# Kernel optimization log

Hardware: AMD Instinct MI355X
Metric: run time of the kernel (lower is better)

Reference implementation:

```python
import jax, jax.numpy as jnp
import numpy as np

HIDDEN_DIM = 2048
NUM_HEADS = 16
HEAD_DIM = HIDDEN_DIM // NUM_HEADS


def setup_inputs() -> dict:
    key = jax.random.key(0)
    ks = jax.random.split(key, 5)
    B, S, D = 1, 2048, HIDDEN_DIM
    scale = 1.0 / np.sqrt(D)
    return {
        "x": jax.random.normal(ks[0], (B, S, D), dtype=jnp.float32),
        "w_q": jax.random.normal(ks[1], (D, D), dtype=jnp.float32) * scale,
        "w_k": jax.random.normal(ks[2], (D, D), dtype=jnp.float32) * scale,
        "w_v": jax.random.normal(ks[3], (D, D), dtype=jnp.float32) * scale,
        "w_o": jax.random.normal(ks[4], (D, D), dtype=jnp.float32) * scale,
    }


def reference(x, w_q, w_k, w_v, w_o):
    # x: (B, S, D). Projections use x @ W.T as in the torch module.
    B, S, D = x.shape
    H, Hd = NUM_HEADS, HEAD_DIM
    q = (x @ w_q.T).reshape(B, S, H, Hd)
    k = (x @ w_k.T).reshape(B, S, H, Hd)
    v = (x @ w_v.T).reshape(B, S, H, Hd)
    scale = 1.0 / np.sqrt(Hd).astype(np.float32)
    # The tiled online-softmax loop computes exact softmax attention.
    scores = jnp.einsum("bqhd,bkhd->bhqk", q, k) * scale  # (B,H,S,S)
    p = jax.nn.softmax(scores, axis=-1)
    o = jnp.einsum("bhqk,bkhd->bqhd", p, v).reshape(B, S, D)
    return o @ w_o.T
```

## Files before the change

### kernel.cpp

```cpp
#include <hip/hip_runtime.h>
#include <hip/hip_bf16.h>
#include <cstdint>
#include <cstddef>

typedef __bf16 bf16x8 __attribute__((ext_vector_type(8)));
typedef float f32x4 __attribute__((ext_vector_type(4)));
typedef float f32x16 __attribute__((ext_vector_type(16)));
typedef unsigned short u16x8 __attribute__((ext_vector_type(8)));
typedef unsigned short u16x4 __attribute__((ext_vector_type(4)));

#define S_LEN 2048
#define DMODEL 2048
#define NHEADS 16
#define HD 128

__device__ inline unsigned short f2bf(float f) {
  union { float f; unsigned int u; } v; v.f = f;
  unsigned int r = (v.u + 0x7fffu + ((v.u >> 16) & 1u)) >> 16;
  return (unsigned short)r;
}

__device__ __forceinline__ void gload16(const unsigned short* g,
                                        unsigned short* lds) {
  __builtin_amdgcn_global_load_lds(
      (const __attribute__((address_space(1))) void*)g,
      (__attribute__((address_space(3))) void*)lds, 16, 0, 0);
}

__global__ void cast_all(const float* __restrict__ x, const float* __restrict__ wq,
                         const float* __restrict__ wk, const float* __restrict__ wv,
                         const float* __restrict__ wo,
                         unsigned short* __restrict__ out, float qscale) {
  const int b = blockIdx.x;
  const int seg = b >> 12;
  const int i = ((b & 4095) * 256 + threadIdx.x) * 4;
  const float* src = seg == 0 ? x : seg == 1 ? wq : seg == 2 ? wk
                   : seg == 3 ? wv : wo;
  const float scale = (seg == 1) ? qscale : 1.0f;
  unsigned short* dst = out + (size_t)seg * ((size_t)S_LEN * DMODEL);
  float4 v = *(const float4*)(src + i);
  u16x4 o;
  o.x = f2bf(v.x * scale); o.y = f2bf(v.y * scale);
  o.z = f2bf(v.z * scale); o.w = f2bf(v.w * scale);
  *(u16x4*)(dst + i) = o;
}

template <int MODE>
__device__ __forceinline__ void gemm_core64(
    const unsigned short* __restrict__ A, const unsigned short* __restrict__ B,
    unsigned short* __restrict__ Cb,
    int M, int N, int K, int m0, int n0,
    unsigned short* As, unsigned short* Bs) {
  constexpr int BK = 64;
  const int tid = threadIdx.x;
  const int wave = tid >> 6, lane = tid & 63;
  const int lg = lane >> 4, lr = lane & 15;
  const int rw = (wave >> 1) * 64;
  const int cw = (wave & 1) * 64;
  const int swz = lr & 7;

  const unsigned short* Ap[4];
  const unsigned short* Bp[4];
  unsigned short *as[4], *bs[4];
#pragma unroll
  for (int j = 0; j < 4; j++) {
    const int cc = j * 256 + tid;
    const int row = cc >> 3;
    const int col8 = (cc & 7) ^ (row & 7);
    Ap[j] = A + (size_t)(m0 + row) * K + col8 * 8;
    Bp[j] = B + (size_t)(n0 + row) * K + col8 * 8;
    as[j] = As + j * 2048 + wave * 512;
    bs[j] = Bs + j * 2048 + wave * 512;
  }

  f32x4 acc[4][4];
#pragma unroll
  for (int i = 0; i < 4; i++)
#pragma unroll
    for (int j = 0; j < 4; j++) acc[i][j] = (f32x4){0.f, 0.f, 0.f, 0.f};

  const int nk = K / BK;
  for (int kt = 0; kt < nk; ++kt) {
    const int ko = kt * BK;
    __syncthreads();
#pragma unroll
    for (int j = 0; j < 4; j++) {
      gload16(Ap[j] + ko, as[j]);
      gload16(Bp[j] + ko, bs[j]);
    }
    __syncthreads();

#pragma unroll
    for (int kk = 0; kk < 2; kk++) {
      bf16x8 af[4], bfr[4];
#pragma unroll
      for (int mt = 0; mt < 4; mt++)
        af[mt] = *(const bf16x8*)(As + (rw + mt * 16 + lr) * 64 +
                                  (((kk * 4 + lg) ^ swz) * 8));
#pragma unroll
      for (int nt = 0; nt < 4; nt++)
        bfr[nt] = *(const bf16x8*)(Bs + (cw + nt * 16 + lr) * 64 +
                                   (((kk * 4 + lg) ^ swz) * 8));
#pragma unroll
      for (int mt = 0; mt < 4; mt++)
#pragma unroll
        for (int nt = 0; nt < 4; nt++)
          acc[mt][nt] = __builtin_amdgcn_mfma_f32_16x16x32_bf16(
              af[mt], bfr[nt], acc[mt][nt], 0, 0, 0);
    }
  }

#pragma unroll
  for (int mt = 0; mt < 4; mt++)
#pragma unroll
    for (int nt = 0; nt < 4; nt++) {
      const int col = n0 + cw + nt * 16 + lr;
#pragma unroll
      for (int r = 0; r < 4; r++) {
        const int row = m0 + rw + mt * 16 + lg * 4 + r;
        const float v = acc[mt][nt][r];
        if (MODE == 1) Cb[(size_t)row * N + col] = f2bf(v);
        else Cb[(size_t)col * M + row] = f2bf(v);
      }
    }
}

__global__ __launch_bounds__(256, 2) void gemm_qkv(
    const unsigned short* __restrict__ xb, const unsigned short* __restrict__ wqb,
    const unsigned short* __restrict__ wkb, const unsigned short* __restrict__ wvb,
    unsigned short* __restrict__ qb, unsigned short* __restrict__ kb,
    unsigned short* __restrict__ vTb) {
  __shared__ unsigned short As[128 * 64];
  __shared__ unsigned short Bs[128 * 64];
  const int which = blockIdx.x >> 4;
  const int n0 = (blockIdx.x & 15) * 128;
  const int m0 = blockIdx.y * 128;
  if (which == 0)
    gemm_core64<1>(xb, wqb, qb, S_LEN, DMODEL, DMODEL, m0, n0, As, Bs);
  else if (which == 1)
    gemm_core64<1>(xb, wkb, kb, S_LEN, DMODEL, DMODEL, m0, n0, As, Bs);
  else
    gemm_core64<2>(xb, wvb, vTb, S_LEN, DMODEL, DMODEL, m0, n0, As, Bs);
}

__global__ __launch_bounds__(256, 2) void gemm_bt64(
    const unsigned short* __restrict__ A, const unsigned short* __restrict__ B,
    float* __restrict__ Cf, int M, int N, int K) {
  constexpr int BK = 128;
  __shared__ unsigned short As[64 * 128];
  __shared__ unsigned short Bs[128 * 128];
  const int tid = threadIdx.x;
  const int wave = tid >> 6, lane = tid & 63;
  const int lg = lane >> 4, lr = lane & 15;
  const int rw = (wave >> 1) * 32;
  const int cw = (wave & 1) * 64;
  const int m0 = blockIdx.y * 64, n0 = blockIdx.x * 128;
  const int swz = lr & 7;

  const unsigned short* Ap[4];
  const unsigned short* Bp[8];
  unsigned short *as[4], *bs[8];
#pragma unroll
  for (int j = 0; j < 4; j++) {
    const int cc = j * 256 + tid;
    const int row = cc >> 4;
    const int col16 = (cc & 15) ^ (row & 7);
    Ap[j] = A + (size_t)(m0 + row) * K + col16 * 8;
    as[j] = As + j * 2048 + wave * 512;
  }
#pragma unroll
  for (int j = 0; j < 8; j++) {
    const int cc = j * 256 + tid;
    const int row = cc >> 4;
    const int col16 = (cc & 15) ^ (row & 7);
    Bp[j] = B + (size_t)(n0 + row) * K + col16 * 8;
    bs[j] = Bs + j * 2048 + wave * 512;
  }

  f32x4 acc[2][4];
#pragma unroll
  for (int i = 0; i < 2; i++)
#pragma unroll
    for (int j = 0; j < 4; j++) acc[i][j] = (f32x4){0.f, 0.f, 0.f, 0.f};

  const int nk = K / BK;
  for (int kt = 0; kt < nk; ++kt) {
    const int ko = kt * BK;
    __syncthreads();
#pragma unroll
    for (int j = 0; j < 4; j++) gload16(Ap[j] + ko, as[j]);
#pragma unroll
    for (int j = 0; j < 8; j++) gload16(Bp[j] + ko, bs[j]);
    __syncthreads();

#pragma unroll
    for (int kk = 0; kk < 4; kk++) {
      bf16x8 af[2], bfr[4];
#pragma unroll
      for (int mt = 0; mt < 2; mt++)
        af[mt] = *(const bf16x8*)(As + (rw + mt * 16 + lr) * 128 +
                                  (((kk * 4 + lg) ^ swz) * 8));
#pragma unroll
      for (int nt = 0; nt < 4; nt++)
        bfr[nt] = *(const bf16x8*)(Bs + (cw + nt * 16 + lr) * 128 +
                                   (((kk * 4 + lg) ^ swz) * 8));
#pragma unroll
      for (int mt = 0; mt < 2; mt++)
#pragma unroll
        for (int nt = 0; nt < 4; nt++)
          acc[mt][nt] = __builtin_amdgcn_mfma_f32_16x16x32_bf16(
              af[mt], bfr[nt], acc[mt][nt], 0, 0, 0);
    }
  }

#pragma unroll
  for (int mt = 0; mt < 2; mt++)
#pragma unroll
    for (int nt = 0; nt < 4; nt++) {
      const int col = n0 + cw + nt * 16 + lr;
#pragma unroll
      for (int r = 0; r < 4; r++) {
        const int row = m0 + rw + mt * 16 + lg * 4 + r;
        Cf[(size_t)row * N + col] = acc[mt][nt][r];
      }
    }
}

__global__ __launch_bounds__(256, 2) void attn_kernel(
    const unsigned short* __restrict__ q, const unsigned short* __restrict__ k,
    const unsigned short* __restrict__ vT, unsigned short* __restrict__ o) {
  constexpr int KT = 64;
  __shared__ unsigned short Ks[2][64 * 136];
  __shared__ unsigned short Vt[128 * 72];
  __shared__ unsigned short Ps[64 * 72];
  __shared__ float Lred[4][32];

  const int tid = threadIdx.x;
  const int w = tid >> 6, lane = tid & 63;
  const int l32 = lane & 31, lh = lane >> 5;
  const int qh = w >> 1;
  const int kh = w & 1;
  const int h = blockIdx.y;
  const int q0 = blockIdx.x * 64;

  bf16x8 qf[8];
#pragma unroll
  for (int ks = 0; ks < 8; ks++)
    qf[ks] = *(const bf16x8*)(q + (size_t)(q0 + qh * 32 + l32) * DMODEL +
                              h * HD + ks * 16 + lh * 8);

  f32x16 Oacc[2];
#pragma unroll
  for (int mt = 0; mt < 2; mt++)
#pragma unroll
    for (int j = 0; j < 16; j++) Oacc[mt][j] = 0.f;
  f32x4 lsumv = (f32x4){0.f, 0.f, 0.f, 0.f};

  int krow[4], kcg[4], vrow[4], vcg[4];
#pragma unroll
  for (int i = 0; i < 4; i++) {
    const int c = i * 256 + tid;
    krow[i] = c >> 4; kcg[i] = c & 15;
    vrow[i] = c >> 3; vcg[i] = c & 7;
  }

  u16x8 kreg[4], vreg[4];
#pragma unroll
  for (int i = 0; i < 4; i++) {
    kreg[i] = *(const u16x8*)(k + (size_t)(krow[i]) * DMODEL + h * HD + kcg[i] * 8);
    vreg[i] = *(const u16x8*)(vT + (size_t)(h * HD + vrow[i]) * S_LEN + vcg[i] * 8);
  }
#pragma unroll
  for (int i = 0; i < 4; i++)
    *(u16x8*)(Ks[0] + krow[i] * 136 + kcg[i] * 8) = kreg[i];
  __syncthreads();

  constexpr int NT = S_LEN / KT;
  for (int kt = 0; kt < NT; ++kt) {
#pragma unroll
    for (int i = 0; i < 4; i++)
      *(u16x8*)(Vt + vrow[i] * 72 + vcg[i] * 8) = vreg[i];

    if (kt + 1 < NT) {
      const int kbase = (kt + 1) * KT;
#pragma unroll
      for (int i = 0; i < 4; i++) {
        kreg[i] = *(const u16x8*)(k + (size_t)(kbase + krow[i]) * DMODEL +
                                  h * HD + kcg[i] * 8);
        vreg[i] = *(const u16x8*)(vT + (size_t)(h * HD + vrow[i]) * S_LEN +
                                  kbase + vcg[i] * 8);
      }
    }

    const unsigned short* Kcur = Ks[kt & 1];
    bf16x8 kf[8];
#pragma unroll
    for (int ks = 0; ks < 8; ks++)
      kf[ks] = *(const bf16x8*)(Kcur + (kh * 32 + l32) * 136 + ks * 16 + lh * 8);

    f32x16 sacc0, sacc1;
#pragma unroll
    for (int j = 0; j < 16; j++) { sacc0[j] = 0.f; sacc1[j] = 0.f; }
    __builtin_amdgcn_s_setprio(1);
#pragma unroll
    for (int ks = 0; ks < 4; ks++) {
      sacc0 = __builtin_amdgcn_mfma_f32_32x32x16_bf16(kf[ks], qf[ks], sacc0,
                                                      0, 0, 0);
      sacc1 = __builtin_amdgcn_mfma_f32_32x32x16_bf16(kf[ks + 4], qf[ks + 4],
                                                      sacc1, 0, 0, 0);
    }
    __builtin_amdgcn_s_setprio(0);
    const f32x16 sacc = sacc0 + sacc1;

#pragma unroll
    for (int rq = 0; rq < 4; rq++) {
      u16x4 pk;
#pragma unroll
      for (int ri = 0; ri < 4; ri++) {
        const float p = __builtin_amdgcn_exp2f(sacc[rq * 4 + ri]);
        lsumv[ri] += p;
        union { float f; unsigned int u; } cv; cv.f = p;
        pk[ri] = (unsigned short)(cv.u >> 16);
      }
      *(u16x4*)(Ps + (qh * 32 + l32) * 72 + kh * 32 + rq * 8 + lh * 4) = pk;
    }

    if (kt + 1 < NT) {
#pragma unroll
      for (int i = 0; i < 4; i++)
        *(u16x8*)(Ks[(kt + 1) & 1] + krow[i] * 136 + kcg[i] * 8) = kreg[i];
    }
    __syncthreads();

    bf16x8 pfr[4], vf[2][4];
#pragma unroll
    for (int ks2 = 0; ks2 < 4; ks2++)
      pfr[ks2] =
          *(const bf16x8*)(Ps + (qh * 32 + l32) * 72 + ks2 * 16 + lh * 8);
#pragma unroll
    for (int ks2 = 0; ks2 < 4; ks2++)
#pragma unroll
      for (int mt = 0; mt < 2; mt++)
        vf[mt][ks2] = *(const bf16x8*)(
            Vt + (kh * 64 + mt * 32 + l32) * 72 + ks2 * 16 + lh * 8);

    __builtin_amdgcn_s_setprio(1);
#pragma unroll
    for (int ks2 = 0; ks2 < 4; ks2++)
#pragma unroll
      for (int mt = 0; mt < 2; mt++)
        Oacc[mt] = __builtin_amdgcn_mfma_f32_32x32x16_bf16(
            vf[mt][ks2], pfr[ks2], Oacc[mt], 0, 0, 0);
    __builtin_amdgcn_s_setprio(0);
    __syncthreads();
  }

  float lsum = (lsumv[0] + lsumv[1]) + (lsumv[2] + lsumv[3]);
  lsum += __shfl_xor(lsum, 32);
  if (lh == 0) Lred[w][l32] = lsum;
  __syncthreads();
  const float ltot = Lred[qh * 2][l32] + Lred[qh * 2 + 1][l32];
  const float inv = 1.0f / ltot;

#pragma unroll
  for (int mt = 0; mt < 2; mt++)
#pragma unroll
    for (int rq = 0; rq < 4; rq++) {
      u16x4 pk;
#pragma unroll
      for (int ri = 0; ri < 4; ri++)
        pk[ri] = f2bf(Oacc[mt][rq * 4 + ri] * inv);
      *(u16x4*)(Ks[0] + (qh * 32 + l32) * 136 + kh * 64 + mt * 32 + rq * 8 +
                lh * 4) = pk;
    }
  __syncthreads();
#pragma unroll
  for (int i = 0; i < 4; i++) {
    const int c = i * 256 + tid;
    const int row = c >> 4, ch = c & 15;
    const u16x8 vv = *(const u16x8*)(Ks[0] + row * 136 + ch * 8);
    *(u16x8*)(o + (size_t)(q0 + row) * DMODEL + h * HD + ch * 8) = vv;
  }
}

extern "C" void kernel_launch(void* const* d_in, const int* in_sizes, int n_in,
                              void* d_out, int out_size, void* d_ws, size_t ws_size,
                              hipStream_t stream) {
  (void)in_sizes; (void)n_in; (void)out_size; (void)ws_size;
  const float* x  = (const float*)d_in[0];
  const float* wq = (const float*)d_in[1];
  const float* wk = (const float*)d_in[2];
  const float* wv = (const float*)d_in[3];
  const float* wo = (const float*)d_in[4];
  float* out = (float*)d_out;

  const size_t NE = (size_t)S_LEN * DMODEL;
  unsigned short* ws = (unsigned short*)d_ws;
  unsigned short* xb  = ws + 0 * NE;
  unsigned short* wqb = ws + 1 * NE;
  unsigned short* wkb = ws + 2 * NE;
  unsigned short* wvb = ws + 3 * NE;
  unsigned short* wob = ws + 4 * NE;
  unsigned short* qb  = ws + 5 * NE;
  unsigned short* kb  = ws + 6 * NE;
  unsigned short* vTb = ws + 7 * NE;
  unsigned short* ob  = ws + 8 * NE;

  const float qscale = 0.08838834764831845f * 1.4426950408889634f;

  cast_all<<<dim3(5 * 4096), dim3(256), 0, stream>>>(x, wq, wk, wv, wo, ws,
                                                     qscale);

  gemm_qkv<<<dim3(48, 16), dim3(256), 0, stream>>>(xb, wqb, wkb, wvb, qb, kb,
                                                   vTb);

  attn_kernel<<<dim3(S_LEN / 64, NHEADS), dim3(256), 0, stream>>>(qb, kb, vTb,
                                                                  ob);

  gemm_bt64<<<dim3(16, 32), dim3(256), 0, stream>>>(ob, wob, out, S_LEN,
                                                    DMODEL, DMODEL);
}
```

Before: 251.3 us.

## Keep P in registers via permlane swap, split keys across waves, swizzle LDS

```diff
diff --git a/kernel.cpp b/kernel.cpp
--- a/kernel.cpp
+++ b/kernel.cpp
@@ -231,13 +231,13 @@
     const unsigned short* __restrict__ vT, unsigned short* __restrict__ o) {
   constexpr int KT = 64;
   __shared__ unsigned short Ks[2][64 * 136];
-  __shared__ unsigned short Vt[128 * 72];
-  __shared__ unsigned short Ps[64 * 72];
+  __shared__ unsigned short Vt[2][128 * 72];
   __shared__ float Lred[4][32];
 
   const int tid = threadIdx.x;
   const int w = tid >> 6, lane = tid & 63;
   const int l32 = lane & 31, lh = lane >> 5;
+  const int l7 = l32 & 7;
   const int qh = w >> 1;
   const int kh = w & 1;
   const int h = blockIdx.y;
@@ -249,20 +249,33 @@
     qf[ks] = *(const bf16x8*)(q + (size_t)(q0 + qh * 32 + l32) * DMODEL +
                               h * HD + ks * 16 + lh * 8);
 
-  f32x16 Oacc[2];
-#pragma unroll
-  for (int mt = 0; mt < 2; mt++)
+  f32x16 Oacc[4];
+#pragma unroll
+  for (int mt = 0; mt < 4; mt++)
 #pragma unroll
     for (int j = 0; j < 16; j++) Oacc[mt][j] = 0.f;
   f32x4 lsumv = (f32x4){0.f, 0.f, 0.f, 0.f};
 
-  int krow[4], kcg[4], vrow[4], vcg[4];
+  int krow[4], kcg[4], vrow[4], vcg[4], kso[4], vso[4];
 #pragma unroll
   for (int i = 0; i < 4; i++) {
     const int c = i * 256 + tid;
     krow[i] = c >> 4; kcg[i] = c & 15;
     vrow[i] = c >> 3; vcg[i] = c & 7;
-  }
+    kso[i] = krow[i] * 136 + (kcg[i] ^ (krow[i] & 7)) * 8;
+    vso[i] = vrow[i] * 72 + (vcg[i] ^ (vrow[i] & 7)) * 8;
+  }
+
+  int kfo[8];
+#pragma unroll
+  for (int ks = 0; ks < 8; ks++)
+    kfo[ks] = (kh * 32 + l32) * 136 + (((ks * 2 + lh) ^ l7) * 8);
+  int vfo[4][2];
+#pragma unroll
+  for (int mt = 0; mt < 4; mt++)
+#pragma unroll
+    for (int s = 0; s < 2; s++)
+      vfo[mt][s] = (mt * 32 + l32) * 72 + (((kh * 4 + s * 2 + lh) ^ l7) * 8);
 
   u16x8 kreg[4], vreg[4];
 #pragma unroll
@@ -271,16 +284,14 @@
     vreg[i] = *(const u16x8*)(vT + (size_t)(h * HD + vrow[i]) * S_LEN + vcg[i] * 8);
   }
 #pragma unroll
-  for (int i = 0; i < 4; i++)
-    *(u16x8*)(Ks[0] + krow[i] * 136 + kcg[i] * 8) = kreg[i];
+  for (int i = 0; i < 4; i++) {
+    *(u16x8*)(Ks[0] + kso[i]) = kreg[i];
+    *(u16x8*)(Vt[0] + vso[i]) = vreg[i];
+  }
   __syncthreads();
 
   constexpr int NT = S_LEN / KT;
   for (int kt = 0; kt < NT; ++kt) {
-#pragma unroll
-    for (int i = 0; i < 4; i++)
-      *(u16x8*)(Vt + vrow[i] * 72 + vcg[i] * 8) = vreg[i];
-
     if (kt + 1 < NT) {
       const int kbase = (kt + 1) * KT;
 #pragma unroll
@@ -292,93 +303,105 @@
       }
     }
 
-    const unsigned short* Kcur = Ks[kt & 1];
-    bf16x8 kf[8];
-#pragma unroll
-    for (int ks = 0; ks < 8; ks++)
-      kf[ks] = *(const bf16x8*)(Kcur + (kh * 32 + l32) * 136 + ks * 16 + lh * 8);
-
+    const unsigned short* Kb = Ks[kt & 1];
     f32x16 sacc0, sacc1;
 #pragma unroll
     for (int j = 0; j < 16; j++) { sacc0[j] = 0.f; sacc1[j] = 0.f; }
     __builtin_amdgcn_s_setprio(1);
 #pragma unroll
     for (int ks = 0; ks < 4; ks++) {
-      sacc0 = __builtin_amdgcn_mfma_f32_32x32x16_bf16(kf[ks], qf[ks], sacc0,
-                                                      0, 0, 0);
-      sacc1 = __builtin_amdgcn_mfma_f32_32x32x16_bf16(kf[ks + 4], qf[ks + 4],
-                                                      sacc1, 0, 0, 0);
+      const bf16x8 kf0 = *(const bf16x8*)(Kb + kfo[ks]);
+      const bf16x8 kf1 = *(const bf16x8*)(Kb + kfo[ks + 4]);
+      sacc0 = __builtin_amdgcn_mfma_f32_32x32x16_bf16(kf0, qf[ks], sacc0, 0, 0, 0);
+      sacc1 = __builtin_amdgcn_mfma_f32_32x32x16_bf16(kf1, qf[ks + 4], sacc1, 0, 0, 0);
     }
     __builtin_amdgcn_s_setprio(0);
     const f32x16 sacc = sacc0 + sacc1;
 
-#pragma unroll
-    for (int rq = 0; rq < 4; rq++) {
-      u16x4 pk;
-#pragma unroll
-      for (int ri = 0; ri < 4; ri++) {
-        const float p = __builtin_amdgcn_exp2f(sacc[rq * 4 + ri]);
-        lsumv[ri] += p;
-        union { float f; unsigned int u; } cv; cv.f = p;
-        pk[ri] = (unsigned short)(cv.u >> 16);
+    float p[16];
+#pragma unroll
+    for (int r = 0; r < 16; r++) p[r] = __builtin_amdgcn_exp2f(sacc[r]);
+#pragma unroll
+    for (int r = 0; r < 4; r++)
+      lsumv[r] += (p[4 * r] + p[4 * r + 1]) + (p[4 * r + 2] + p[4 * r + 3]);
+
+    unsigned int Aw[8];
+#pragma unroll
+    for (int i = 0; i < 8; i++)
+      asm("v_cvt_pk_bf16_f32 %0, %1, %2"
+          : "=v"(Aw[i]) : "v"(p[2 * i]), "v"(p[2 * i + 1]));
+    asm volatile("v_permlane32_swap_b32 %0, %1" : "+v"(Aw[0]), "+v"(Aw[2]));
+    asm volatile("v_permlane32_swap_b32 %0, %1" : "+v"(Aw[1]), "+v"(Aw[3]));
+    asm volatile("v_permlane32_swap_b32 %0, %1" : "+v"(Aw[4]), "+v"(Aw[6]));
+    asm volatile("v_permlane32_swap_b32 %0, %1" : "+v"(Aw[5]), "+v"(Aw[7]));
+    union { unsigned int wd[4]; bf16x8 v; } u0, u1;
+    u0.wd[0] = Aw[0]; u0.wd[1] = Aw[1]; u0.wd[2] = Aw[2]; u0.wd[3] = Aw[3];
+    u1.wd[0] = Aw[4]; u1.wd[1] = Aw[5]; u1.wd[2] = Aw[6]; u1.wd[3] = Aw[7];
+    const bf16x8 pfr0 = u0.v, pfr1 = u1.v;
+
+    const unsigned short* Vb = Vt[kt & 1];
+    __builtin_amdgcn_s_setprio(1);
+#pragma unroll
+    for (int mt = 0; mt < 4; mt++) {
+      const bf16x8 v0 = *(const bf16x8*)(Vb + vfo[mt][0]);
+      const bf16x8 v1 = *(const bf16x8*)(Vb + vfo[mt][1]);
+      Oacc[mt] = __builtin_amdgcn_mfma_f32_32x32x16_bf16(v0, pfr0, Oacc[mt], 0, 0, 0);
+      Oacc[mt] = __builtin_amdgcn_mfma_f32_32x32x16_bf16(v1, pfr1, Oacc[mt], 0, 0, 0);
+    }
+    __builtin_amdgcn_s_setprio(0);
+
+    if (kt + 1 < NT) {
+      unsigned short* Kn = Ks[(kt + 1) & 1];
+      unsigned short* Vn = Vt[(kt + 1) & 1];
+#pragma unroll
+      for (int i = 0; i < 4; i++) {
+        *(u16x8*)(Kn + kso[i]) = kreg[i];
+        *(u16x8*)(Vn + vso[i]) = vreg[i];
       }
-      *(u16x4*)(Ps + (qh * 32 + l32) * 72 + kh * 32 + rq * 8 + lh * 4) = pk;
-    }
-
-    if (kt + 1 < NT) {
-#pragma unroll
-      for (int i = 0; i < 4; i++)
-        *(u16x8*)(Ks[(kt + 1) & 1] + krow[i] * 136 + kcg[i] * 8) = kreg[i];
-    }
-    __syncthreads();
-
-    bf16x8 pfr[4], vf[2][4];
-#pragma unroll
-    for (int ks2 = 0; ks2 < 4; ks2++)
-      pfr[ks2] =
-          *(const bf16x8*)(Ps + (qh * 32 + l32) * 72 + ks2 * 16 + lh * 8);
-#pragma unroll
-    for (int ks2 = 0; ks2 < 4; ks2++)
-#pragma unroll
-      for (int mt = 0; mt < 2; mt++)
-        vf[mt][ks2] = *(const bf16x8*)(
-            Vt + (kh * 64 + mt * 32 + l32) * 72 + ks2 * 16 + lh * 8);
-
-    __builtin_amdgcn_s_setprio(1);
-#pragma unroll
-    for (int ks2 = 0; ks2 < 4; ks2++)
-#pragma unroll
-      for (int mt = 0; mt < 2; mt++)
-        Oacc[mt] = __builtin_amdgcn_mfma_f32_32x32x16_bf16(
-            vf[mt][ks2], pfr[ks2], Oacc[mt], 0, 0, 0);
-    __builtin_amdgcn_s_setprio(0);
+    }
     __syncthreads();
   }
 
   float lsum = (lsumv[0] + lsumv[1]) + (lsumv[2] + lsumv[3]);
   lsum += __shfl_xor(lsum, 32);
   if (lh == 0) Lred[w][l32] = lsum;
+
+  float* Of = (float*)(&Ks[0][0]);
+  if (kh == 1) {
+#pragma unroll
+    for (int mt = 0; mt < 4; mt++)
+#pragma unroll
+      for (int r = 0; r < 16; r++)
+        Of[qh * 4096 + mt * 1024 + r * 64 + lh * 32 + l32] = Oacc[mt][r];
+  }
   __syncthreads();
-  const float ltot = Lred[qh * 2][l32] + Lred[qh * 2 + 1][l32];
-  const float inv = 1.0f / ltot;
-
-#pragma unroll
-  for (int mt = 0; mt < 2; mt++)
-#pragma unroll
-    for (int rq = 0; rq < 4; rq++) {
-      u16x4 pk;
-#pragma unroll
-      for (int ri = 0; ri < 4; ri++)
-        pk[ri] = f2bf(Oacc[mt][rq * 4 + ri] * inv);
-      *(u16x4*)(Ks[0] + (qh * 32 + l32) * 136 + kh * 64 + mt * 32 + rq * 8 +
-                lh * 4) = pk;
-    }
+
+  unsigned short* Tb = &Vt[0][0];
+  if (kh == 0) {
+    const float ltot = Lred[qh * 2][l32] + Lred[qh * 2 + 1][l32];
+    const float inv = 1.0f / ltot;
+#pragma unroll
+    for (int mt = 0; mt < 4; mt++)
+#pragma unroll
+      for (int rq = 0; rq < 4; rq++) {
+        u16x4 pk;
+#pragma unroll
+        for (int ri = 0; ri < 4; ri++) {
+          const int r = rq * 4 + ri;
+          const float v = Oacc[mt][r] +
+              Of[qh * 4096 + mt * 1024 + r * 64 + lh * 32 + l32];
+          pk[ri] = f2bf(v * inv);
+        }
+        *(u16x4*)(Tb + (qh * 32 + l32) * 136 + mt * 32 + rq * 8 + lh * 4) = pk;
+      }
+  }
   __syncthreads();
+
 #pragma unroll
   for (int i = 0; i < 4; i++) {
     const int c = i * 256 + tid;
     const int row = c >> 4, ch = c & 15;
-    const u16x8 vv = *(const u16x8*)(Ks[0] + row * 136 + ch * 8);
+    const u16x8 vv = *(const u16x8*)(Tb + row * 136 + ch * 8);
     *(u16x8*)(o + (size_t)(q0 + row) * DMODEL + h * HD + ch * 8) = vv;
   }
 }
```

New measurement: 251.8 us. Within noise of the previous version (+0.2%).
